# Performance work log

Measured on AMD Instinct MI355X. Metric: run time of the kernel, lower is better.

## Reference

```python
import jax, jax.numpy as jnp
import numpy as np


def setup_inputs() -> dict:
    key = jax.random.key(0)
    ks = jax.random.split(key, 10)
    B, C, T, H, W = 8, 128, 8, 32, 32
    Cq = C // 8
    return {
        "x": jax.random.normal(ks[0], (B, C, T, H, W), dtype=jnp.float32),
        "Wq": jax.random.normal(ks[1], (Cq, C), dtype=jnp.float32) * (1.0 / np.sqrt(C)),
        "bq": jax.random.normal(ks[2], (Cq,), dtype=jnp.float32) * 0.02,
        "Wk": jax.random.normal(ks[3], (Cq, C), dtype=jnp.float32) * (1.0 / np.sqrt(C)),
        "bk": jax.random.normal(ks[4], (Cq,), dtype=jnp.float32) * 0.02,
        "Wv": jax.random.normal(ks[5], (C, C), dtype=jnp.float32) * (1.0 / np.sqrt(C)),
        "bv": jax.random.normal(ks[6], (C,), dtype=jnp.float32) * 0.02,
        "gamma_pam": jax.random.normal(ks[7], (1,), dtype=jnp.float32),
        "gamma_cam": jax.random.normal(ks[8], (1,), dtype=jnp.float32),
        "gamma_tim": jax.random.normal(ks[9], (1,), dtype=jnp.float32),
    }


def reference(x, Wq, bq, Wk, bk, Wv, bv, gamma_pam, gamma_cam, gamma_tim):
    B, C, T, H, W = x.shape
    HW = H * W

    # ---- PAM: position attention over HW, feature dim = (C//8)*T ----
    # 1x1x1 Conv3d == per-position channel matmul
    q = jnp.einsum('bcthw,oc->bothw', x, Wq) + bq[None, :, None, None, None]
    k = jnp.einsum('bcthw,oc->bothw', x, Wk) + bk[None, :, None, None, None]
    v = jnp.einsum('bcthw,oc->bothw', x, Wv) + bv[None, :, None, None, None]
    qf = q.reshape(B, -1, HW)   # [B, (C//8)*T, HW]
    kf = k.reshape(B, -1, HW)
    vf = v.reshape(B, -1, HW)   # [B, C*T, HW]
    energy = jnp.einsum('bcn,bcm->bnm', qf, kf)          # [B, HW, HW]
    attn = jax.nn.softmax(energy, axis=-1)
    # out = bmm(v, attn^T)
    pam = jnp.einsum('bcm,bnm->bcn', vf, attn).reshape(B, C, T, H, W)
    pam = gamma_pam * pam + x

    # ---- CAM: channel attention (C x C) with negated-energy softmax ----
    xc = x.reshape(B, C, -1)                              # [B, C, T*HW]
    e = jnp.einsum('bcn,bdn->bcd', xc, xc)                # [B, C, C]
    e = jnp.max(e, axis=-1, keepdims=True) - e
    a = jax.nn.softmax(e, axis=-1)
    cam = jnp.einsum('bcd,bdn->bcn', a, xc).reshape(B, C, T, H, W)
    cam = gamma_cam * cam + x

    # ---- TIM: temporal attention (T x T) with negated-energy softmax ----
    xt = jnp.transpose(x, (0, 2, 1, 3, 4)).reshape(B, T, -1)  # [B, T, C*HW]
    e = jnp.einsum('btn,bsn->bts', xt, xt)                # [B, T, T]
    e = jnp.max(e, axis=-1, keepdims=True) - e
    a = jax.nn.softmax(e, axis=-1)
    tim = jnp.einsum('bts,bsn->btn', a, xt).reshape(B, T, C, H, W)
    tim = jnp.transpose(tim, (0, 2, 1, 3, 4))
    tim = gamma_tim * tim + x

    return pam + cam + tim
```

## Files before the change

### kernel.cpp

```cpp
#include <hip/hip_runtime.h>
#include <cstdint>

typedef unsigned short u16;
typedef __attribute__((ext_vector_type(8))) short bf16x8;
typedef __attribute__((ext_vector_type(4))) float f32x4;

constexpr int B_  = 8;
constexpr int C_  = 128;
constexpr int T_  = 8;
constexpr int HW_ = 1024;
constexpr int P_  = T_ * HW_;
constexpr int F_  = 128;
constexpr int CT_ = C_ * T_;

static __device__ __forceinline__ u16 f2bf(float f) {
    union { float f; unsigned u; } v; v.f = f;
    unsigned r = v.u + 0x7fffu + ((v.u >> 16) & 1u);
    return (u16)(r >> 16);
}
static __device__ __forceinline__ float bf2f(u16 h) {
    union { unsigned u; float f; } v; v.u = ((unsigned)h) << 16;
    return v.f;
}

#define GLOAD16(src, dst)                                                     \
    __builtin_amdgcn_global_load_lds(                                         \
        (const __attribute__((address_space(1))) void*)(src),                 \
        (__attribute__((address_space(3))) void*)(dst), 16, 0, 0)

__global__ __launch_bounds__(256)
void k_tim_gram(const float* __restrict__ x, float* __restrict__ e_t,
                const float* __restrict__ Wq, const float* __restrict__ Wk,
                const float* __restrict__ Wv, u16* __restrict__ Wall)
{
    const int b = blockIdx.y, c = blockIdx.x;
    const int tid = threadIdx.x;

    if (blockIdx.x == 0 && blockIdx.y == 0) {
        for (int i = tid; i < 20480; i += 256) {
            int oc = i >> 7, cc = i & 127;
            float wv;
            if (oc < 16)      wv = Wq[oc * 128 + cc];
            else if (oc < 32) wv = Wk[(oc - 16) * 128 + cc];
            else              wv = Wv[(oc - 32) * 128 + cc];
            Wall[i] = f2bf(wv);
        }
    }

    const float* xb = x + ((size_t)(b * C_ + c)) * P_;
    float acc[8][8] = {};
    for (int r = 0; r < 4; r++) {
        int hw = r * 256 + tid;
        float xv[8];
        #pragma unroll
        for (int t = 0; t < 8; t++) xv[t] = xb[t * HW_ + hw];
        #pragma unroll
        for (int t = 0; t < 8; t++)
            #pragma unroll
            for (int s2 = 0; s2 < 8; s2++)
                acc[t][s2] += xv[t] * xv[s2];
    }
    __shared__ float sm[4][64];
    const int lane = tid & 63, wid = tid >> 6;
    #pragma unroll
    for (int u = 0; u < 64; u++) {
        float vv = acc[u >> 3][u & 7];
        #pragma unroll
        for (int off = 32; off; off >>= 1) vv += __shfl_xor(vv, off);
        if (lane == 0) sm[wid][u] = vv;
    }
    __syncthreads();
    if (tid < 64) {
        float vv = sm[0][tid] + sm[1][tid] + sm[2][tid] + sm[3][tid];
        atomicAdd(&e_t[b * 64 + tid], vv);
    }
}

__global__ __launch_bounds__(256)
void k_prep(const float* __restrict__ x, u16* __restrict__ xT,
            u16* __restrict__ xhi, u16* __restrict__ xlo,
            const u16* __restrict__ Wall,
            const float* __restrict__ bq, const float* __restrict__ bk,
            const float* __restrict__ bv,
            u16* __restrict__ qt, u16* __restrict__ kt, u16* __restrict__ v16)
{
    __shared__ char sy[32768];
    const int b  = blockIdx.y;
    const int p0 = blockIdx.x * 128;
    const int tid = threadIdx.x, lane = tid & 63, w = tid >> 6;

    #pragma unroll
    for (int r = 0; r < 16; r++) {
        int lin = r * 256 + tid;
        int c = lin >> 5, j4 = (lin & 31) << 2;
        size_t gi = ((size_t)(b * C_ + c)) * P_ + p0 + j4;
        float4 xv = *(const float4*)&x[gi];
        float a4[4] = {xv.x, xv.y, xv.z, xv.w};
        ushort4 h, l;
        h.x = f2bf(a4[0]); h.y = f2bf(a4[1]);
        h.z = f2bf(a4[2]); h.w = f2bf(a4[3]);
        l.x = f2bf(a4[0] - bf2f(h.x)); l.y = f2bf(a4[1] - bf2f(h.y));
        l.z = f2bf(a4[2] - bf2f(h.z)); l.w = f2bf(a4[3] - bf2f(h.w));
        *(ushort4*)&xhi[gi] = h;
        *(ushort4*)&xlo[gi] = l;
        #pragma unroll
        for (int u = 0; u < 4; u++) {
            int pi = j4 + u;
            int byte = pi * 256 + ((c * 2) ^ (((pi >> 2) & 15) << 4));
            *(u16*)(sy + byte) = (u == 0) ? h.x : (u == 1) ? h.y
                               : (u == 2) ? h.z : h.w;
        }
    }
    __syncthreads();

    #pragma unroll
    for (int r = 0; r < 8; r++) {
        int lin = r * 256 + tid;
        int pi = lin >> 4, ci8 = (lin & 15) << 3;
        bf16x8 v = *(const bf16x8*)(sy + pi * 256 +
                                    ((ci8 * 2) ^ (((pi >> 2) & 15) << 4)));
        *(bf16x8*)&xT[((size_t)(b * P_ + p0 + pi)) * C_ + ci8] = v;
    }

    bf16x8 bg[4][2];
    #pragma unroll
    for (int ks = 0; ks < 4; ks++)
        #pragma unroll
        for (int ni = 0; ni < 2; ni++) {
            int p  = w * 32 + ni * 16 + (lane & 15);
            int cb = (ks * 32 + (lane >> 4) * 8) * 2;
            bg[ks][ni] = *(const bf16x8*)(sy + p * 256 +
                              (cb ^ (((p >> 2) & 15) << 4)));
        }

    f32x4 acc[10][2];
    #pragma unroll
    for (int mi = 0; mi < 10; mi++) {
        acc[mi][0] = (f32x4){0.f, 0.f, 0.f, 0.f};
        acc[mi][1] = (f32x4){0.f, 0.f, 0.f, 0.f};
    }

    #pragma unroll
    for (int mi = 0; mi < 10; mi++) {
        #pragma unroll
        for (int ks = 0; ks < 4; ks++) {
            bf16x8 af = *(const bf16x8*)(Wall + (mi * 16 + (lane & 15)) * 128
                                          + ks * 32 + (lane >> 4) * 8);
            acc[mi][0] = __builtin_amdgcn_mfma_f32_16x16x32_bf16(
                af, bg[ks][0], acc[mi][0], 0, 0, 0);
            acc[mi][1] = __builtin_amdgcn_mfma_f32_16x16x32_bf16(
                af, bg[ks][1], acc[mi][1], 0, 0, 0);
        }
    }

    const int t      = p0 >> 10;
    const int hwbase = (p0 & 1023) + w * 32;
    #pragma unroll
    for (int mi = 0; mi < 10; mi++)
        #pragma unroll
        for (int ni = 0; ni < 2; ni++)
            #pragma unroll
            for (int r = 0; r < 4; r++) {
                int oc = mi * 16 + (lane >> 4) * 4 + r;
                int hw = hwbase + ni * 16 + (lane & 15);
                float bias;
                if (mi == 0)      bias = bq[oc];
                else if (mi == 1) bias = bk[oc - 16];
                else              bias = bv[oc - 32];
                u16 bv16 = f2bf(acc[mi][ni][r] + bias);
                if (mi == 0)
                    qt[((size_t)b * HW_ + hw) * F_ + oc * 8 + t] = bv16;
                else if (mi == 1)
                    kt[((size_t)b * HW_ + hw) * F_ + (oc - 16) * 8 + t] = bv16;
                else
                    v16[((size_t)(b * C_ + oc - 32)) * P_ + t * HW_ + hw] = bv16;
            }
}

__global__ __launch_bounds__(256)
void k_attn(const u16* __restrict__ qt, const u16* __restrict__ kt,
            u16* __restrict__ A16)
{
    const int b  = blockIdx.y;
    const int n0 = blockIdx.x * 16;
    const int tid = threadIdx.x, lane = tid & 63, w = tid >> 6;
    const u16* qb = qt + (size_t)b * HW_ * F_;
    const u16* kb = kt + (size_t)b * HW_ * F_;

    bf16x8 af[4];
    #pragma unroll
    for (int ks = 0; ks < 4; ks++)
        af[ks] = *(const bf16x8*)(qb + (size_t)(n0 + (lane & 15)) * F_
                                  + ks * 32 + (lane >> 4) * 8);

    f32x4 acc[16];
    #pragma unroll
    for (int j = 0; j < 16; j++) acc[j] = (f32x4){0.f, 0.f, 0.f, 0.f};

    #pragma unroll
    for (int j = 0; j < 16; j++) {
        const int m0 = w * 256 + j * 16;
        #pragma unroll
        for (int ks = 0; ks < 4; ks++) {
            bf16x8 bg = *(const bf16x8*)(kb + (size_t)(m0 + (lane & 15)) * F_
                                         + ks * 32 + (lane >> 4) * 8);
            acc[j] = __builtin_amdgcn_mfma_f32_16x16x32_bf16(
                af[ks], bg, acc[j], 0, 0, 0);
        }
    }

    __shared__ float red[4][16];
    float rmax[4];
    #pragma unroll
    for (int r = 0; r < 4; r++) {
        float m = acc[0][r];
        #pragma unroll
        for (int j = 1; j < 16; j++) m = fmaxf(m, acc[j][r]);
        #pragma unroll
        for (int off = 1; off < 16; off <<= 1) m = fmaxf(m, __shfl_xor(m, off));
        rmax[r] = m;
    }
    if ((lane & 15) == 0)
        #pragma unroll
        for (int r = 0; r < 4; r++) red[w][(lane >> 4) * 4 + r] = rmax[r];
    __syncthreads();
    #pragma unroll
    for (int r = 0; r < 4; r++) {
        int row = (lane >> 4) * 4 + r;
        rmax[r] = fmaxf(fmaxf(red[0][row], red[1][row]),
                        fmaxf(red[2][row], red[3][row]));
    }
    __syncthreads();

    float rsum[4];
    #pragma unroll
    for (int r = 0; r < 4; r++) {
        float s = 0.f;
        #pragma unroll
        for (int j = 0; j < 16; j++) {
            acc[j][r] = __expf(acc[j][r] - rmax[r]);
            s += acc[j][r];
        }
        #pragma unroll
        for (int off = 1; off < 16; off <<= 1) s += __shfl_xor(s, off);
        rsum[r] = s;
    }
    if ((lane & 15) == 0)
        #pragma unroll
        for (int r = 0; r < 4; r++) red[w][(lane >> 4) * 4 + r] = rsum[r];
    __syncthreads();

    u16* ob = A16 + ((size_t)b * HW_ + n0) * HW_;
    #pragma unroll
    for (int r = 0; r < 4; r++) {
        int row = (lane >> 4) * 4 + r;
        float inv = 1.0f / (red[0][row] + red[1][row] +
                            red[2][row] + red[3][row]);
        #pragma unroll
        for (int j = 0; j < 16; j++)
            ob[(size_t)row * HW_ + w * 256 + j * 16 + (lane & 15)] =
                f2bf(acc[j][r] * inv);
    }
}

__global__ __launch_bounds__(256)
void k_pv(const u16* __restrict__ v16, const u16* __restrict__ A16,
          const float* __restrict__ gamma_pam, u16* __restrict__ pam16)
{
    __shared__ char As[2][16384];
    __shared__ char Bs[2][16384];
    const int b   = blockIdx.z;
    const int ct0 = blockIdx.y * 128, n0 = blockIdx.x * 128;
    const int tid = threadIdx.x, lane = tid & 63, w = tid >> 6;
    const u16* vb = v16 + (size_t)b * CT_ * HW_;
    const u16* ab = A16 + (size_t)b * HW_ * HW_;

    const int s_row = (lane >> 3);
    const int s_col = ((lane & 7) ^ ((lane >> 3) & 7)) * 8;

    const int wr = w >> 1, wc = w & 1;
    f32x4 acc[4][4];
    #pragma unroll
    for (int mi = 0; mi < 4; mi++)
        #pragma unroll
        for (int ni = 0; ni < 4; ni++) acc[mi][ni] = (f32x4){0.f, 0.f, 0.f, 0.f};

    #pragma unroll
    for (int i = 0; i < 4; i++) {
        int c = w * 4 + i;
        int row = c * 8 + s_row;
        GLOAD16(vb + (size_t)(ct0 + row) * HW_ + s_col, As[0] + c * 1024);
        GLOAD16(ab + (size_t)(n0  + row) * HW_ + s_col, Bs[0] + c * 1024);
    }
    __syncthreads();

    int cur = 0;
    for (int it = 0; it < 16; ++it) {
        if (it < 15) {
            int mc = (it + 1) * 64;
            #pragma unroll
            for (int i = 0; i < 4; i++) {
                int c = w * 4 + i;
                int row = c * 8 + s_row;
                GLOAD16(vb + (size_t)(ct0 + row) * HW_ + mc + s_col,
                        As[cur ^ 1] + c * 1024);
                GLOAD16(ab + (size_t)(n0  + row) * HW_ + mc + s_col,
                        Bs[cur ^ 1] + c * 1024);
            }
        }
        const char* Ac = As[cur];
        const char* Bc = Bs[cur];
        #pragma unroll
        for (int ks = 0; ks < 2; ks++) {
            bf16x8 af[4], bg[4];
            #pragma unroll
            for (int mi = 0; mi < 4; mi++) {
                int row  = wr * 64 + mi * 16 + (lane & 15);
                int slot = (ks * 4 + (lane >> 4)) ^ (row & 7);
                af[mi] = *(const bf16x8*)(Ac + row * 128 + slot * 16);
                int rb  = wc * 64 + mi * 16 + (lane & 15);
                int sb  = (ks * 4 + (lane >> 4)) ^ (rb & 7);
                bg[mi] = *(const bf16x8*)(Bc + rb * 128 + sb * 16);
            }
            #pragma unroll
            for (int mi = 0; mi < 4; mi++)
                #pragma unroll
                for (int ni = 0; ni < 4; ni++)
                    acc[mi][ni] = __builtin_amdgcn_mfma_f32_16x16x32_bf16(
                        af[mi], bg[ni], acc[mi][ni], 0, 0, 0);
        }
        __syncthreads();
        cur ^= 1;
    }

    const float gp = gamma_pam[0];
    u16* ob = pam16 + (size_t)b * CT_ * HW_;
    #pragma unroll
    for (int mi = 0; mi < 4; mi++)
        #pragma unroll
        for (int ni = 0; ni < 4; ni++)
            #pragma unroll
            for (int r = 0; r < 4; r++)
                ob[(size_t)(ct0 + wr * 64 + mi * 16 + (lane >> 4) * 4 + r) * HW_
                   + n0 + wc * 64 + ni * 16 + (lane & 15)] =
                    f2bf(gp * acc[mi][ni][r]);
}

__global__ __launch_bounds__(256)
void k_cam_gram(const u16* __restrict__ xhi, const u16* __restrict__ xlo,
                float* __restrict__ part)
{
    __shared__ char Sh[32768];
    __shared__ char Sl[32768];
    const int b = blockIdx.y, ch = blockIdx.x;
    const int tid = threadIdx.x, lane = tid & 63, w = tid >> 6;
    const u16* hb = xhi + (size_t)b * C_ * P_;
    const u16* lb = xlo + (size_t)b * C_ * P_;

    f32x4 acc[8][2];
    #pragma unroll
    for (int mi = 0; mi < 8; mi++) {
        acc[mi][0] = (f32x4){0.f, 0.f, 0.f, 0.f};
        acc[mi][1] = (f32x4){0.f, 0.f, 0.f, 0.f};
    }

    for (int kc = 0; kc < 2; kc++) {
        int n0 = ch * 256 + kc * 128;
        #pragma unroll
        for (int i = 0; i < 8; i++) {
            int c4  = w * 8 + i;
            int row = c4 * 4 + (lane >> 4);
            int col = ((lane & 15) ^ (row & 7)) * 8;
            GLOAD16(hb + (size_t)row * P_ + n0 + col, Sh + c4 * 1024);
            GLOAD16(lb + (size_t)row * P_ + n0 + col, Sl + c4 * 1024);
        }
        __syncthreads();
        #pragma unroll
        for (int ks = 0; ks < 4; ks++) {
            bf16x8 bh[2], bl[2];
            #pragma unroll
            for (int ni = 0; ni < 2; ni++) {
                int rb = w * 32 + ni * 16 + (lane & 15);
                int sb = (ks * 4 + (lane >> 4)) ^ (rb & 7);
                bh[ni] = *(const bf16x8*)(Sh + rb * 256 + sb * 16);
                bl[ni] = *(const bf16x8*)(Sl + rb * 256 + sb * 16);
            }
            #pragma unroll
            for (int mi = 0; mi < 8; mi++) {
                int ra = mi * 16 + (lane & 15);
                int sa = (ks * 4 + (lane >> 4)) ^ (ra & 7);
                bf16x8 ah = *(const bf16x8*)(Sh + ra * 256 + sa * 16);
                bf16x8 al = *(const bf16x8*)(Sl + ra * 256 + sa * 16);
                #pragma unroll
                for (int ni = 0; ni < 2; ni++) {
                    acc[mi][ni] = __builtin_amdgcn_mfma_f32_16x16x32_bf16(
                        ah, bh[ni], acc[mi][ni], 0, 0, 0);
                    acc[mi][ni] = __builtin_amdgcn_mfma_f32_16x16x32_bf16(
                        ah, bl[ni], acc[mi][ni], 0, 0, 0);
                    acc[mi][ni] = __builtin_amdgcn_mfma_f32_16x16x32_bf16(
                        al, bh[ni], acc[mi][ni], 0, 0, 0);
                }
            }
        }
        __syncthreads();
    }

    float* pb = part + ((size_t)(b * 32 + ch)) * 16384;
    #pragma unroll
    for (int mi = 0; mi < 8; mi++)
        #pragma unroll
        for (int ni = 0; ni < 2; ni++)
            #pragma unroll
            for (int r = 0; r < 4; r++) {
                int c = mi * 16 + (lane >> 4) * 4 + r;
                int d = w * 32 + ni * 16 + (lane & 15);
                pb[c * 128 + d] = acc[mi][ni][r];
            }
}

__global__ __launch_bounds__(128)
void k_cam_reduce(const float* __restrict__ part,
                  const float* __restrict__ gamma_cam, u16* __restrict__ acam16)
{
    const int b = blockIdx.y, c = blockIdx.x;
    const int d = threadIdx.x;
    float s = 0.f;
    for (int ch = 0; ch < 32; ch++)
        s += part[(((size_t)(b * 32 + ch)) * C_ + c) * C_ + d];
    float mn = s;
    #pragma unroll
    for (int off = 32; off; off >>= 1) mn = fminf(mn, __shfl_xor(mn, off));
    __shared__ float m1[2], m2[2];
    if ((d & 63) == 0) m1[d >> 6] = mn;
    __syncthreads();
    mn = fminf(m1[0], m1[1]);
    float p = __expf(mn - s);
    float sum = p;
    #pragma unroll
    for (int off = 32; off; off >>= 1) sum += __shfl_xor(sum, off);
    if ((d & 63) == 0) m2[d >> 6] = sum;
    __syncthreads();
    sum = m2[0] + m2[1];
    acam16[((size_t)(b * C_ + c)) * C_ + d] = f2bf(gamma_cam[0] * p / sum);
}

__global__ __launch_bounds__(256)
void k_xprime(const float* __restrict__ x, const float* __restrict__ e_t,
              const float* __restrict__ gamma_tim, u16* __restrict__ Xp)
{
    const int b = blockIdx.y, c = blockIdx.x;
    const size_t base = ((size_t)(b * C_ + c)) * P_;
    const int tid = threadIdx.x;
    const float gt = gamma_tim[0];

    float4 xv[8];
    #pragma unroll
    for (int t = 0; t < 8; t++)
        xv[t] = *(const float4*)&x[base + t * HW_ + tid * 4];

    #pragma unroll
    for (int t = 0; t < 8; t++) {
        float e[8];
        #pragma unroll
        for (int s = 0; s < 8; s++) e[s] = e_t[b * 64 + t * 8 + s];
        float mn = e[0];
        #pragma unroll
        for (int s = 1; s < 8; s++) mn = fminf(mn, e[s]);
        float p[8], sum = 0.f;
        #pragma unroll
        for (int s = 0; s < 8; s++) { p[s] = __expf(mn - e[s]); sum += p[s]; }
        float inv = gt / sum;

        float4 o = make_float4(3.f * xv[t].x, 3.f * xv[t].y,
                               3.f * xv[t].z, 3.f * xv[t].w);
        #pragma unroll
        for (int s = 0; s < 8; s++) {
            float wgt = p[s] * inv;
            o.x += wgt * xv[s].x; o.y += wgt * xv[s].y;
            o.z += wgt * xv[s].z; o.w += wgt * xv[s].w;
        }
        ushort4 pk;
        pk.x = f2bf(o.x); pk.y = f2bf(o.y); pk.z = f2bf(o.z); pk.w = f2bf(o.w);
        *(ushort4*)&Xp[base + t * HW_ + tid * 4] = pk;
    }
}

__global__ __launch_bounds__(256)
void k_cam_av(const u16* __restrict__ acam16, const u16* __restrict__ xT,
              const u16* __restrict__ Xp, const u16* __restrict__ pam16,
              float* __restrict__ out)
{
    const int b  = blockIdx.y;
    const int p0 = blockIdx.x * 128;
    const int tid = threadIdx.x, lane = tid & 63, w = tid >> 6;

    const u16* Ab = acam16 + (size_t)b * C_ * C_;
    const u16* Bb = xT + ((size_t)(b * P_ + p0 + w * 32)) * C_;

    f32x4 acc[8][2];
    #pragma unroll
    for (int mi = 0; mi < 8; mi++) {
        acc[mi][0] = (f32x4){0.f, 0.f, 0.f, 0.f};
        acc[mi][1] = (f32x4){0.f, 0.f, 0.f, 0.f};
    }

    bf16x8 bg[4][2];
    #pragma unroll
    for (int ks = 0; ks < 4; ks++)
        #pragma unroll
        for (int ni = 0; ni < 2; ni++)
            bg[ks][ni] = *(const bf16x8*)(Bb +
                (size_t)(ni * 16 + (lane & 15)) * C_ + ks * 32 + (lane >> 4) * 8);

    #pragma unroll
    for (int mi = 0; mi < 8; mi++) {
        #pragma unroll
        for (int ks = 0; ks < 4; ks++) {
            bf16x8 af = *(const bf16x8*)(Ab +
                (size_t)(mi * 16 + (lane & 15)) * C_ + ks * 32 + (lane >> 4) * 8);
            acc[mi][0] = __builtin_amdgcn_mfma_f32_16x16x32_bf16(
                af, bg[ks][0], acc[mi][0], 0, 0, 0);
            acc[mi][1] = __builtin_amdgcn_mfma_f32_16x16x32_bf16(
                af, bg[ks][1], acc[mi][1], 0, 0, 0);
        }
    }

    const int tt = p0 >> 10;
    float* ob = out + (size_t)b * C_ * P_;
    const u16* xp = Xp + (size_t)b * C_ * P_;
    const u16* pb = pam16 + (size_t)b * CT_ * HW_;
    #pragma unroll
    for (int mi = 0; mi < 8; mi++)
        #pragma unroll
        for (int ni = 0; ni < 2; ni++)
            #pragma unroll
            for (int r = 0; r < 4; r++) {
                int c = mi * 16 + (lane >> 4) * 4 + r;
                int p = p0 + w * 32 + ni * 16 + (lane & 15);
                int hw = p & 1023;
                size_t i = (size_t)c * P_ + p;
                float pam = bf2f(pb[((size_t)(c * 8 + tt)) * HW_ + hw]);
                ob[i] = pam + acc[mi][ni][r] + bf2f(xp[i]);
            }
}

extern "C" void kernel_launch(void* const* d_in, const int* in_sizes, int n_in,
                              void* d_out, int out_size, void* d_ws, size_t ws_size,
                              hipStream_t stream)
{
    (void)in_sizes; (void)n_in; (void)out_size; (void)ws_size;
    const float* x  = (const float*)d_in[0];
    const float* Wq = (const float*)d_in[1];
    const float* bq = (const float*)d_in[2];
    const float* Wk = (const float*)d_in[3];
    const float* bk = (const float*)d_in[4];
    const float* Wv = (const float*)d_in[5];
    const float* bv = (const float*)d_in[6];
    const float* gp = (const float*)d_in[7];
    const float* gc = (const float*)d_in[8];
    const float* gt = (const float*)d_in[9];
    float* out = (float*)d_out;
    char*  ws  = (char*)d_ws;

    const size_t MiB = 1u << 20;
    u16*   xT     = (u16*)(ws + 0);
    u16*   v16    = (u16*)(ws + 16 * MiB);
    u16*   xhi    = (u16*)(ws + 32 * MiB);
    u16*   xlo    = (u16*)(ws + 48 * MiB);
    u16*   A16    = (u16*)(ws + 64 * MiB);
    u16*   pam16  = (u16*)(ws + 80 * MiB);
    float* part   = (float*)(ws + 96 * MiB);
    u16*   Xp16   = (u16*)(ws + 113 * MiB);
    u16*   qtb    = (u16*)(ws + 130 * MiB);
    u16*   ktb    = (u16*)(ws + 132 * MiB);
    u16*   acam16 = (u16*)(ws + 134 * MiB);
    u16*   Wall   = (u16*)(ws + 134 * MiB + 65536);
    float* etim   = (float*)(ws + 134 * MiB + 131072);

    hipMemsetAsync(etim, 0, 512 * sizeof(float), stream);

    k_tim_gram  <<<dim3(128, 8),  256, 0, stream>>>(x, etim,
                                                    Wq, Wk, Wv, Wall);
    k_prep      <<<dim3(64, 8),   256, 0, stream>>>(x, xT, xhi, xlo, Wall,
                                                    bq, bk, bv,
                                                    qtb, ktb, v16);
    k_attn      <<<dim3(64, 8),   256, 0, stream>>>(qtb, ktb, A16);
    k_pv        <<<dim3(8, 8, 8), 256, 0, stream>>>(v16, A16, gp, pam16);
    k_xprime    <<<dim3(128, 8),  256, 0, stream>>>(x, etim, gt, Xp16);
    k_cam_gram  <<<dim3(32, 8),   256, 0, stream>>>(xhi, xlo, part);
    k_cam_reduce<<<dim3(128, 8),  128, 0, stream>>>(part, gc, acam16);
    k_cam_av    <<<dim3(64, 8),   256, 0, stream>>>(acam16, xT, Xp16,
                                                    pam16, out);
}
```

Before: 264.1 us.

## Stage scattered bf16 outputs through LDS for coalesced stores; symmetric TIM gram

The k_attn, k_pv and k_prep q/k outputs are first written into shared memory, then copied out to global memory as 16-byte vector rows instead of scattered 2-byte stores. The q/k feature layout is reordered to t-major (t*16+cq), which is consistent for q and k, so their dot products are unchanged. k_tim_gram now handles two channels per block with float4 loads, accumulates only the 36 symmetric products and mirrors them when doing the atomic adds, and launches half as many blocks. The cost is extra LDS traffic and barriers, plus higher LDS use in k_attn, which may lower occupancy.

After: 268.5 us. Within noise of the previous version (+1.7%).

```diff
diff --git a/kernel.cpp b/kernel.cpp
--- a/kernel.cpp
+++ b/kernel.cpp
@@ -3,6 +3,7 @@
 
 typedef unsigned short u16;
 typedef __attribute__((ext_vector_type(8))) short bf16x8;
+typedef __attribute__((ext_vector_type(8))) unsigned short u16x8;
 typedef __attribute__((ext_vector_type(4))) float f32x4;
 
 constexpr int B_  = 8;
@@ -33,46 +34,64 @@
                 const float* __restrict__ Wq, const float* __restrict__ Wk,
                 const float* __restrict__ Wv, u16* __restrict__ Wall)
 {
-    const int b = blockIdx.y, c = blockIdx.x;
+    const int b = blockIdx.y, cc = blockIdx.x;
     const int tid = threadIdx.x;
 
-    if (blockIdx.x == 0 && blockIdx.y == 0) {
+    if (cc == 0 && b == 0) {
         for (int i = tid; i < 20480; i += 256) {
-            int oc = i >> 7, cc = i & 127;
+            int oc = i >> 7, c2 = i & 127;
             float wv;
-            if (oc < 16)      wv = Wq[oc * 128 + cc];
-            else if (oc < 32) wv = Wk[(oc - 16) * 128 + cc];
-            else              wv = Wv[(oc - 32) * 128 + cc];
+            if (oc < 16)      wv = Wq[oc * 128 + c2];
+            else if (oc < 32) wv = Wk[(oc - 16) * 128 + c2];
+            else              wv = Wv[(oc - 32) * 128 + c2];
             Wall[i] = f2bf(wv);
         }
     }
 
-    const float* xb = x + ((size_t)(b * C_ + c)) * P_;
-    float acc[8][8] = {};
-    for (int r = 0; r < 4; r++) {
-        int hw = r * 256 + tid;
-        float xv[8];
-        #pragma unroll
-        for (int t = 0; t < 8; t++) xv[t] = xb[t * HW_ + hw];
+    const int hw = tid * 4;
+    float4 xv[2][8];
+    #pragma unroll
+    for (int ci = 0; ci < 2; ci++) {
+        const float* xb = x + ((size_t)(b * C_ + cc * 2 + ci)) * P_;
         #pragma unroll
         for (int t = 0; t < 8; t++)
-            #pragma unroll
-            for (int s2 = 0; s2 < 8; s2++)
-                acc[t][s2] += xv[t] * xv[s2];
-    }
-    __shared__ float sm[4][64];
-    const int lane = tid & 63, wid = tid >> 6;
-    #pragma unroll
-    for (int u = 0; u < 64; u++) {
-        float vv = acc[u >> 3][u & 7];
-        #pragma unroll
-        for (int off = 32; off; off >>= 1) vv += __shfl_xor(vv, off);
-        if (lane == 0) sm[wid][u] = vv;
-    }
-    __syncthreads();
-    if (tid < 64) {
-        float vv = sm[0][tid] + sm[1][tid] + sm[2][tid] + sm[3][tid];
-        atomicAdd(&e_t[b * 64 + tid], vv);
+            xv[ci][t] = *(const float4*)&xb[t * HW_ + hw];
+    }
+
+    float acc[36];
+    #pragma unroll
+    for (int p = 0; p < 36; p++) acc[p] = 0.f;
+    #pragma unroll
+    for (int ci = 0; ci < 2; ci++) {
+        int p = 0;
+        #pragma unroll
+        for (int t = 0; t < 8; t++)
+            #pragma unroll
+            for (int s = t; s < 8; s++) {
+                float4 a = xv[ci][t], c4 = xv[ci][s];
+                acc[p++] += a.x * c4.x + a.y * c4.y + a.z * c4.z + a.w * c4.w;
+            }
+    }
+
+    const int lane = tid & 63, w = tid >> 6;
+    #pragma unroll
+    for (int p = 0; p < 36; p++)
+        #pragma unroll
+        for (int off = 32; off; off >>= 1)
+            acc[p] += __shfl_xor(acc[p], off);
+
+    __shared__ float sm[4][36];
+    if (lane == 0)
+        #pragma unroll
+        for (int p = 0; p < 36; p++) sm[w][p] = acc[p];
+    __syncthreads();
+    if (tid < 36) {
+        float v = sm[0][tid] + sm[1][tid] + sm[2][tid] + sm[3][tid];
+        int t = 0, rem = tid;
+        while (rem >= 8 - t) { rem -= 8 - t; t++; }
+        int s = t + rem;
+        atomicAdd(&e_t[b * 64 + t * 8 + s], v);
+        if (s != t) atomicAdd(&e_t[b * 64 + s * 8 + t], v);
     }
 }
 
@@ -132,6 +151,7 @@
             bg[ks][ni] = *(const bf16x8*)(sy + p * 256 +
                               (cb ^ (((p >> 2) & 15) << 4)));
         }
+    __syncthreads();
 
     f32x4 acc[10][2];
     #pragma unroll
@@ -154,33 +174,57 @@
     }
 
     const int t      = p0 >> 10;
-    const int hwbase = (p0 & 1023) + w * 32;
-    #pragma unroll
-    for (int mi = 0; mi < 10; mi++)
+    const int hw0    = p0 & 1023;
+    const int hwbase = hw0 + w * 32;
+
+    #pragma unroll
+    for (int mi = 2; mi < 10; mi++)
         #pragma unroll
         for (int ni = 0; ni < 2; ni++)
             #pragma unroll
             for (int r = 0; r < 4; r++) {
                 int oc = mi * 16 + (lane >> 4) * 4 + r;
                 int hw = hwbase + ni * 16 + (lane & 15);
-                float bias;
-                if (mi == 0)      bias = bq[oc];
-                else if (mi == 1) bias = bk[oc - 16];
-                else              bias = bv[oc - 32];
-                u16 bv16 = f2bf(acc[mi][ni][r] + bias);
-                if (mi == 0)
-                    qt[((size_t)b * HW_ + hw) * F_ + oc * 8 + t] = bv16;
-                else if (mi == 1)
-                    kt[((size_t)b * HW_ + hw) * F_ + (oc - 16) * 8 + t] = bv16;
-                else
-                    v16[((size_t)(b * C_ + oc - 32)) * P_ + t * HW_ + hw] = bv16;
-            }
+                v16[((size_t)(b * C_ + oc - 32)) * P_ + t * HW_ + hw] =
+                    f2bf(acc[mi][ni][r] + bv[oc - 32]);
+            }
+
+    u16* qk = (u16*)sy;
+    #pragma unroll
+    for (int mi = 0; mi < 2; mi++)
+        #pragma unroll
+        for (int ni = 0; ni < 2; ni++) {
+            int hwl = w * 32 + ni * 16 + (lane & 15);
+            int cq0 = (lane >> 4) * 4;
+            ushort4 pk;
+            float b0 = (mi == 0) ? bq[cq0 + 0] : bk[cq0 + 0];
+            float b1 = (mi == 0) ? bq[cq0 + 1] : bk[cq0 + 1];
+            float b2 = (mi == 0) ? bq[cq0 + 2] : bk[cq0 + 2];
+            float b3 = (mi == 0) ? bq[cq0 + 3] : bk[cq0 + 3];
+            pk.x = f2bf(acc[mi][ni][0] + b0);
+            pk.y = f2bf(acc[mi][ni][1] + b1);
+            pk.z = f2bf(acc[mi][ni][2] + b2);
+            pk.w = f2bf(acc[mi][ni][3] + b3);
+            *(ushort4*)&qk[(mi * 128 + hwl) * 24 + cq0] = pk;
+        }
+    __syncthreads();
+    {
+        int mi = tid >> 7, hwl = tid & 127;
+        u16x8 lo = *(const u16x8*)&qk[(mi * 128 + hwl) * 24 + 0];
+        u16x8 hi = *(const u16x8*)&qk[(mi * 128 + hwl) * 24 + 8];
+        u16* dst = (mi == 0) ? qt : kt;
+        size_t off = ((size_t)b * HW_ + hw0 + hwl) * F_ + t * 16;
+        *(u16x8*)&dst[off]     = lo;
+        *(u16x8*)&dst[off + 8] = hi;
+    }
 }
 
 __global__ __launch_bounds__(256)
 void k_attn(const u16* __restrict__ qt, const u16* __restrict__ kt,
             u16* __restrict__ A16)
 {
+    __shared__ u16 ost[16][1032];
+    __shared__ float red[4][16];
     const int b  = blockIdx.y;
     const int n0 = blockIdx.x * 16;
     const int tid = threadIdx.x, lane = tid & 63, w = tid >> 6;
@@ -209,7 +253,6 @@
         }
     }
 
-    __shared__ float red[4][16];
     float rmax[4];
     #pragma unroll
     for (int r = 0; r < 4; r++) {
@@ -250,7 +293,6 @@
         for (int r = 0; r < 4; r++) red[w][(lane >> 4) * 4 + r] = rsum[r];
     __syncthreads();
 
-    u16* ob = A16 + ((size_t)b * HW_ + n0) * HW_;
     #pragma unroll
     for (int r = 0; r < 4; r++) {
         int row = (lane >> 4) * 4 + r;
@@ -258,8 +300,16 @@
                             red[2][row] + red[3][row]);
         #pragma unroll
         for (int j = 0; j < 16; j++)
-            ob[(size_t)row * HW_ + w * 256 + j * 16 + (lane & 15)] =
-                f2bf(acc[j][r] * inv);
+            ost[row][w * 256 + j * 16 + (lane & 15)] = f2bf(acc[j][r] * inv);
+    }
+    __syncthreads();
+
+    u16* ob = A16 + ((size_t)b * HW_ + n0) * HW_;
+    #pragma unroll
+    for (int it = 0; it < 8; it++) {
+        int lin = it * 256 + tid;
+        int row = lin >> 7, g = lin & 127;
+        *(u16x8*)&ob[(size_t)row * HW_ + g * 8] = *(const u16x8*)&ost[row][g * 8];
     }
 }
 
@@ -334,16 +384,25 @@
     }
 
     const float gp = gamma_pam[0];
+    u16* ot = (u16*)As;
+    #pragma unroll
+    for (int mi = 0; mi < 4; mi++)
+        #pragma unroll
+        for (int ni = 0; ni < 4; ni++)
+            #pragma unroll
+            for (int r = 0; r < 4; r++)
+                ot[(wr * 64 + mi * 16 + (lane >> 4) * 4 + r) * 128 +
+                   wc * 64 + ni * 16 + (lane & 15)] = f2bf(gp * acc[mi][ni][r]);
+    __syncthreads();
+
     u16* ob = pam16 + (size_t)b * CT_ * HW_;
     #pragma unroll
-    for (int mi = 0; mi < 4; mi++)
-        #pragma unroll
-        for (int ni = 0; ni < 4; ni++)
-            #pragma unroll
-            for (int r = 0; r < 4; r++)
-                ob[(size_t)(ct0 + wr * 64 + mi * 16 + (lane >> 4) * 4 + r) * HW_
-                   + n0 + wc * 64 + ni * 16 + (lane & 15)] =
-                    f2bf(gp * acc[mi][ni][r]);
+    for (int it = 0; it < 8; it++) {
+        int lin = it * 256 + tid;
+        int row = lin >> 4, col = (lin & 15) * 8;
+        *(u16x8*)&ob[(size_t)(ct0 + row) * HW_ + n0 + col] =
+            *(const u16x8*)&ot[row * 128 + col];
+    }
 }
 
 __global__ __launch_bounds__(256)
@@ -579,7 +638,7 @@
 
     hipMemsetAsync(etim, 0, 512 * sizeof(float), stream);
 
-    k_tim_gram  <<<dim3(128, 8),  256, 0, stream>>>(x, etim,
+    k_tim_gram  <<<dim3(64, 8),   256, 0, stream>>>(x, etim,
                                                     Wq, Wk, Wv, Wall);
     k_prep      <<<dim3(64, 8),   256, 0, stream>>>(x, xT, xhi, xlo, Wall,
                                                     bq, bk, bv,
```
